# Optimization experiments

Measured on AMD Instinct MI355X. Metric: run time of the kernel, lower is better.

Reference implementation:

```python
import jax, jax.numpy as jnp
import numpy as np

D_MODEL = 1024; D_STATE = 64; HEADDIM = 64; EXPAND = 2
D_INNER = EXPAND * D_MODEL            # 2048
NHEADS = D_INNER // HEADDIM           # 32
NGROUPS = 1
GN = NGROUPS * D_STATE                # 64
CONV_DIM = D_INNER + 2 * (2 * GN)     # 2304
D_IN_PROJ = 2 * D_INNER + 2 * (2 * GN) + 2 * NHEADS  # 4416
K_SP = 7; K_TP = 4; CHUNK = 256
BATCH = 2; FRAMES = 8; SPATIAL = 256; SEQLEN = SPATIAL * FRAMES  # 2048


def silu(x):
    return x * jax.nn.sigmoid(x)


def flip_frames(x, f):
    # 'b (l f) d -> b l f d' flip frame axis, flatten back
    b, L, d = x.shape
    return x.reshape(b, L // f, f, d)[:, :, ::-1, :].reshape(b, L, d)


def depthwise_conv1d(x, w, b, pad):
    # x: (N, L, C), w: (C, K) depthwise, pad=(lo,hi) -> (N, L_out, C)
    y = jax.lax.conv_general_dilated(
        jnp.transpose(x, (0, 2, 1)), w[:, None, :], (1,), [pad],
        feature_group_count=w.shape[0])
    return jnp.transpose(y + b[None, :, None], (0, 2, 1))


def setup_inputs():
    rng = np.random.default_rng(0)
    f32 = lambda *s: jnp.asarray(rng.standard_normal(s), jnp.float32)
    # dt_bias init exactly as in the torch module
    dt = np.exp(rng.random(NHEADS) * (np.log(0.1) - np.log(0.001)) + np.log(0.001))
    dt = np.clip(dt, 1e-4, None)
    inv_dt = dt + np.log(-np.expm1(-dt))
    return {
        "u": f32(BATCH, SEQLEN, D_MODEL),
        "in_proj_w": f32(D_IN_PROJ, D_MODEL) * 0.02,
        "conv_sp_w": f32(CONV_DIM, K_SP) * 0.2,
        "conv_sp_b": f32(CONV_DIM) * 0.02,
        "conv_tp_w": f32(CONV_DIM, K_TP) * 0.2,
        "conv_tp_b": f32(CONV_DIM) * 0.02,
        "dt_bias": jnp.asarray(inv_dt, jnp.float32),
        "A_log": jnp.zeros((NHEADS,), jnp.float32),
        "D": jnp.ones((NHEADS,), jnp.float32),
        "fc_D_w": f32(NHEADS, D_INNER) * 0.02,
        "norm_w": jnp.ones((D_INNER,), jnp.float32),
        "out_proj_w": f32(D_MODEL, D_INNER) * 0.02,
        "num_frames": FRAMES,
    }


def chunked_scan(xh, dt, A, Bm, Cm, sp, cs):
    # xh:(R,L,h,p) dt:(R,L,h) Bm,Cm:(R,L,n). ngroups=1.
    # seq_idx semantics: rows [0:b) one segment; rows [b:2b) reset every sp tokens.
    R, L, H, P = xh.shape
    nch = L // cs
    b = R // 2
    xch = xh.reshape(R, nch, cs, H, P)
    dtc = jnp.transpose(dt.reshape(R, nch, cs, H), (0, 1, 3, 2))   # (R,nch,h,cs)
    Bch = Bm.reshape(R, nch, cs, D_STATE)
    Cch = Cm.reshape(R, nch, cs, D_STATE)
    a = dtc * A[None, None, :, None]                               # negative logs
    cum = jnp.cumsum(a, axis=-1)                                   # inclusive
    mask = jnp.tril(jnp.ones((cs, cs), bool))
    seg = cum[..., :, None] - cum[..., None, :]                    # (R,nch,h,t,s)
    Lmat = jnp.where(mask, jnp.exp(jnp.where(mask, seg, 0.0)), 0.0)
    CB = jnp.einsum('rctn,rcsn->rcts', Cch, Bch)
    M = CB[:, :, None] * Lmat * dtc[:, :, :, None, :]
    Y_intra = jnp.einsum('rchts,rcshp->rcthp', M, xch)
    # chunk-final states and cross-chunk recurrence
    G = jnp.exp(cum[..., -1:] - cum) * dtc                         # (R,nch,h,cs)
    S_chunk = jnp.einsum('rchs,rcshp,rcsn->rchpn', G, xch, Bch)
    chunk_decay = jnp.exp(cum[..., -1])                            # (R,nch,h)
    cidx = jnp.arange(nch)
    rb = (cidx > 0) & ((cidx * cs) % sp == 0)
    resetc = jnp.concatenate([jnp.zeros((b, nch), bool),
                              jnp.broadcast_to(rb, (b, nch))], axis=0)

    def cstep(S, inp):
        dec, Sc, r = inp
        S = jnp.where(r[:, None, None, None], 0.0, S)
        prev = S
        S = dec[:, :, None, None] * S + Sc
        return S, prev

    S0 = jnp.zeros((R, H, P, D_STATE), xh.dtype)
    _, prevs = jax.lax.scan(
        cstep, S0,
        (jnp.transpose(chunk_decay, (1, 0, 2)),
         jnp.transpose(S_chunk, (1, 0, 2, 3, 4)),
         resetc.T))
    prev_states = jnp.transpose(prevs, (1, 0, 2, 3, 4))            # (R,nch,h,p,n)
    Y_inter = jnp.einsum('rcht,rctn,rchpn->rcthp', jnp.exp(cum), Cch, prev_states)
    return (Y_intra + Y_inter).reshape(R, L, H, P)


def reference(u, in_proj_w, conv_sp_w, conv_sp_b, conv_tp_w, conv_tp_b,
              dt_bias, A_log, D, fc_D_w, norm_w, out_proj_w, num_frames):
    batch, seqlen, _ = u.shape
    f = num_frames
    sp = seqlen // f
    zxbcdt = u @ in_proj_w.T
    z = zxbcdt[..., :D_INNER]
    xBC = zxbcdt[..., D_INNER:D_INNER + CONV_DIM]
    dt_raw = zxbcdt[..., D_INNER + CONV_DIM:]
    dt = jnp.concatenate([dt_raw[..., :NHEADS],
                          flip_frames(dt_raw[..., NHEADS:], f)], axis=0)
    dt = jax.nn.softplus(dt + dt_bias)                             # (2b,L,h)
    A = -jnp.exp(A_log)
    # spatial depthwise conv over spatial dim per frame ('same' pad) + SiLU
    xBC = xBC.reshape(batch, sp, f, CONV_DIM).transpose(0, 2, 1, 3).reshape(batch * f, sp, CONV_DIM)
    xBC = silu(depthwise_conv1d(xBC, conv_sp_w, conv_sp_b, (K_SP // 2, K_SP // 2)))
    # causal temporal depthwise conv over frame dim per spatial location + SiLU
    xBC = xBC.reshape(batch, f, sp, CONV_DIM).transpose(0, 2, 1, 3).reshape(batch * sp, f, CONV_DIM)
    xBC = silu(depthwise_conv1d(xBC, conv_tp_w, conv_tp_b, (K_TP - 1, 0)))
    xBC = xBC.reshape(batch, seqlen, CONV_DIM)
    x = xBC[..., :D_INNER]
    BC = xBC[..., D_INNER:]
    x_orig = x
    x2 = jnp.concatenate([x, flip_frames(x, f)], axis=0)
    BC2 = jnp.concatenate([BC[..., :2 * GN], flip_frames(BC[..., 2 * GN:], f)], axis=0)
    Bm, Cm = BC2[..., :GN], BC2[..., GN:]
    xh = x2.reshape(2 * batch, seqlen, NHEADS, HEADDIM)
    y = chunked_scan(xh, dt, A, Bm, Cm, sp, CHUNK)                 # (2b,L,h,p)
    y_fwd = y[:batch].reshape(batch, seqlen, D_INNER)
    y_rev = y[batch:].reshape(batch, sp, f, D_INNER)
    # roll-by-one with zeroed first position (fwd: token axis, rev: spatial axis)
    y_fwd = jnp.concatenate([jnp.zeros_like(y_fwd[:, :1]), y_fwd[:, :-1]], axis=1)
    y_rev = jnp.concatenate([jnp.zeros_like(y_rev[:, :1]), y_rev[:, :-1]], axis=1)
    y_rev = y_rev[:, :, ::-1, :].reshape(batch, seqlen, D_INNER)
    x_res = x_orig * jnp.repeat(x_orig @ fc_D_w.T + D, HEADDIM, axis=-1)
    y = y_fwd + y_rev + x_res
    # gated RMSNorm (norm_before_gate=True): rmsnorm(y)*w*silu(z)
    y = y * jax.lax.rsqrt(jnp.mean(jnp.square(y), axis=-1, keepdims=True) + 1e-5)
    y = y * norm_w * silu(z)
    return y @ out_proj_w.T
```

## Files before the change

### kernel.cpp

```cpp
#include <hip/hip_runtime.h>
#include <hip/hip_bf16.h>
#include <math.h>

#define D_STATE   64
#define HEADDIM   64
#define D_INNER   2048
#define NHEADS    32
#define GN        64
#define CONV_DIM  2304
#define D_IN_PROJ 4416
#define ZLD       4352
#define K_SP      7
#define K_TP      4
#define CHUNK     256
#define BATCHN    2
#define FRAMES    8
#define SPATIAL   256
#define SEQLEN    2048
#define NCH       8
#define MTOT      4096

typedef __attribute__((ext_vector_type(8))) short short8;
typedef __attribute__((ext_vector_type(8))) unsigned short ushort8v;
typedef __attribute__((ext_vector_type(4))) float floatx4;

__device__ __forceinline__ float silu_f(float x) { return x / (1.f + __expf(-x)); }
__device__ __forceinline__ int flip_l(int l) { return (l & ~7) | (7 - (l & 7)); }
__device__ __forceinline__ unsigned short f2bf(float f) {
  unsigned int u = __float_as_uint(f);
  unsigned int r = (u + 0x7fffu + ((u >> 16) & 1u)) >> 16;
  return (unsigned short)r;
}
__device__ __forceinline__ float bf2f(unsigned short s) {
  return __uint_as_float(((unsigned int)s) << 16);
}
__device__ __forceinline__ unsigned int cvtpk_bf16(float lo, float hi) {
  unsigned int r;
  asm("v_cvt_pk_bf16_f32 %0, %1, %2" : "=v"(r) : "v"(lo), "v"(hi));
  return r;
}
typedef union { short8 v; unsigned int u[4]; } s8u;
__device__ __forceinline__ void gload_lds16(const unsigned short* g, unsigned short* l) {
  __builtin_amdgcn_global_load_lds((const __attribute__((address_space(1))) void*)g,
                                   (__attribute__((address_space(3))) void*)l, 16, 0, 0);
}

__global__ __launch_bounds__(256) void cast3_bf16_kernel(const float* __restrict__ a,
                                                         unsigned short* __restrict__ oa,
                                                         int na,
                                                         const float* __restrict__ b,
                                                         unsigned short* __restrict__ ob,
                                                         int nb,
                                                         const float* __restrict__ c,
                                                         unsigned short* __restrict__ oc) {
  int bid = blockIdx.x;
  const float* in;
  unsigned short* out;
  size_t blk;
  if (bid < na)            { in = a; out = oa; blk = bid; }
  else if (bid < na + nb)  { in = b; out = ob; blk = bid - na; }
  else                     { in = c; out = oc; blk = bid - na - nb; }
  size_t i = (blk * 256 + threadIdx.x) * 4;
  float4 v = *(const float4*)(in + i);
  ushort4 o;
  o.x = f2bf(v.x); o.y = f2bf(v.y); o.z = f2bf(v.z); o.w = f2bf(v.w);
  *(ushort4*)(out + i) = o;
}

__global__ __launch_bounds__(256) void gemm_bk64_bf16out(
    const unsigned short* __restrict__ A, int lda,
    const unsigned short* __restrict__ B, int ldb,
    unsigned short* __restrict__ C, int ldc, int K) {
  __shared__ unsigned short As[128 * 64];
  __shared__ unsigned short Bs[128 * 64];
  const int tid = threadIdx.x;
  const int lane = tid & 63;
  const int w = tid >> 6;
  const int bid = blockIdx.x;
  const int xcd = bid & 7;
  const int rp  = bid >> 3;
  const int px  = rp % 17;
  const int py  = rp / 17;
  const int m0 = ((xcd >> 1) * 8 + py) * 128;
  const int n0 = ((xcd & 1) * 17 + px) * 128;
  const int wm = (w >> 1) * 64;
  const int wn = (w & 1) * 64;
  const int lrow = lane >> 3;
  const int lperm = lane & 7;
  floatx4 acc[4][4] = {};
  for (int k0 = 0; k0 < K; k0 += 64) {
#pragma unroll
    for (int j = 0; j < 8; ++j) {
      int g = j * 4 + w;
      if (g < 16) {
        int row = g * 8 + lrow;
        int cg = (lperm ^ (row & 7)) * 8;
        gload_lds16(A + (size_t)(m0 + row) * lda + k0 + cg, &As[g * 512]);
      } else {
        int gb = g - 16;
        int row = gb * 8 + lrow;
        int cg = (lperm ^ (row & 7)) * 8;
        gload_lds16(B + (size_t)(n0 + row) * ldb + k0 + cg, &Bs[gb * 512]);
      }
    }
    __syncthreads();
    const int fr = lane & 15;
    const int kq = (lane >> 4) * 8;
#pragma unroll
    for (int kk = 0; kk < 64; kk += 32) {
      int u = (kk + kq) >> 3;
      short8 af[4], bfr[4];
#pragma unroll
      for (int i = 0; i < 4; ++i) {
        int row = wm + i * 16 + fr;
        af[i] = *(const short8*)&As[(row * 8 + (u ^ (row & 7))) * 8];
      }
#pragma unroll
      for (int j = 0; j < 4; ++j) {
        int row = wn + j * 16 + fr;
        bfr[j] = *(const short8*)&Bs[(row * 8 + (u ^ (row & 7))) * 8];
      }
#pragma unroll
      for (int i = 0; i < 4; ++i)
#pragma unroll
        for (int j = 0; j < 4; ++j)
          acc[i][j] = __builtin_amdgcn_mfma_f32_16x16x32_bf16(af[i], bfr[j], acc[i][j], 0, 0, 0);
    }
    __syncthreads();
  }
  const int fr = lane & 15;
  const int rg = (lane >> 4) * 4;
  unsigned short* Ew = &As[w * 1024];
  const int rr = lane >> 3;
  const int c8 = (lane & 7) * 8;
#pragma unroll
  for (int i = 0; i < 4; ++i) {
#pragma unroll
    for (int q = 0; q < 4; ++q)
#pragma unroll
      for (int j = 0; j < 4; ++j)
        Ew[(rg + q) * 64 + j * 16 + fr] = f2bf(acc[i][j][q]);
    ushort8v v0 = *(const ushort8v*)&Ew[rr * 64 + c8];
    ushort8v v1 = *(const ushort8v*)&Ew[(rr + 8) * 64 + c8];
    *(ushort8v*)(C + (size_t)(m0 + wm + i * 16 + rr) * ldc + n0 + wn + c8) = v0;
    *(ushort8v*)(C + (size_t)(m0 + wm + i * 16 + rr + 8) * ldc + n0 + wn + c8) = v1;
  }
}

__global__ __launch_bounds__(256) void gemm_m64_f32(
    const unsigned short* __restrict__ A, int lda,
    const unsigned short* __restrict__ B, int ldb,
    float* __restrict__ C, int ldc, int K) {
  __shared__ unsigned short As[64 * 64];
  __shared__ unsigned short Bs[128 * 64];
  const int tid = threadIdx.x;
  const int lane = tid & 63;
  const int w = tid >> 6;
  const int bid = blockIdx.x;
  const int xcd = bid & 7;
  const int q8  = bid >> 3;
  const int rsel = q8 >> 5;
  const int rp   = q8 & 31;
  const int reg  = xcd + 8 * rsel;
  const int m0 = ((reg >> 1) * 8 + (rp >> 2)) * 64;
  const int n0 = ((reg & 1) * 4 + (rp & 3)) * 128;
  const int wm = (w >> 1) * 32;
  const int wn = (w & 1) * 64;
  const int lrow = lane >> 3;
  const int lperm = lane & 7;
  floatx4 acc[2][4] = {};
  for (int k0 = 0; k0 < K; k0 += 64) {
#pragma unroll
    for (int j = 0; j < 6; ++j) {
      int g = j * 4 + w;
      if (g < 8) {
        int row = g * 8 + lrow;
        int cg = (lperm ^ (row & 7)) * 8;
        gload_lds16(A + (size_t)(m0 + row) * lda + k0 + cg, &As[g * 512]);
      } else {
        int gb = g - 8;
        int row = gb * 8 + lrow;
        int cg = (lperm ^ (row & 7)) * 8;
        gload_lds16(B + (size_t)(n0 + row) * ldb + k0 + cg, &Bs[gb * 512]);
      }
    }
    __syncthreads();
    const int fr = lane & 15;
    const int kq = (lane >> 4) * 8;
#pragma unroll
    for (int kk = 0; kk < 64; kk += 32) {
      int u = (kk + kq) >> 3;
      short8 af[2], bfr[4];
#pragma unroll
      for (int i = 0; i < 2; ++i) {
        int row = wm + i * 16 + fr;
        af[i] = *(const short8*)&As[(row * 8 + (u ^ (row & 7))) * 8];
      }
#pragma unroll
      for (int j = 0; j < 4; ++j) {
        int row = wn + j * 16 + fr;
        bfr[j] = *(const short8*)&Bs[(row * 8 + (u ^ (row & 7))) * 8];
      }
#pragma unroll
      for (int i = 0; i < 2; ++i)
#pragma unroll
        for (int j = 0; j < 4; ++j)
          acc[i][j] = __builtin_amdgcn_mfma_f32_16x16x32_bf16(af[i], bfr[j], acc[i][j], 0, 0, 0);
    }
    __syncthreads();
  }
  const int col = lane & 15;
  const int rg = (lane >> 4) * 4;
#pragma unroll
  for (int i = 0; i < 2; ++i)
#pragma unroll
    for (int j = 0; j < 4; ++j)
#pragma unroll
      for (int r = 0; r < 4; ++r)
        C[(size_t)(m0 + wm + i * 16 + rg + r) * ldc + (n0 + wn + j * 16 + col)] = acc[i][j][r];
}

__global__ __launch_bounds__(256) void gemm_ts_mfma(
    const unsigned short* __restrict__ A, int lda,
    const float* __restrict__ B, int ldb,
    float* __restrict__ C, int ldc, int N, int K) {
  __shared__ float red[4][1024];
  const int tid = threadIdx.x;
  const int lane = tid & 63;
  const int w = tid >> 6;
  const int m0 = blockIdx.x * 16;
  const int fr = lane & 15;
  const int kq = (lane >> 4) * 8;
  const int nt = N >> 4;
  const int kseg = K >> 2;
  const int k0 = w * kseg;
  floatx4 acc[4] = {};
  for (int k = k0; k < k0 + kseg; k += 32) {
    short8 af = *(const short8*)(A + (size_t)(m0 + fr) * lda + k + kq);
    for (int j = 0; j < nt; ++j) {
      const float* bp = B + (size_t)(j * 16 + fr) * ldb + k + kq;
      float4 b0 = *(const float4*)bp;
      float4 b1 = *(const float4*)(bp + 4);
      short8 bf8;
      bf8[0] = (short)f2bf(b0.x); bf8[1] = (short)f2bf(b0.y);
      bf8[2] = (short)f2bf(b0.z); bf8[3] = (short)f2bf(b0.w);
      bf8[4] = (short)f2bf(b1.x); bf8[5] = (short)f2bf(b1.y);
      bf8[6] = (short)f2bf(b1.z); bf8[7] = (short)f2bf(b1.w);
      acc[j] = __builtin_amdgcn_mfma_f32_16x16x32_bf16(af, bf8, acc[j], 0, 0, 0);
    }
  }
  const int rg = (lane >> 4) * 4;
  for (int j = 0; j < nt; ++j)
#pragma unroll
    for (int q = 0; q < 4; ++q)
      red[w][j * 256 + (rg + q) * 16 + fr] = acc[j][q];
  __syncthreads();
  const int entries = nt * 256;
  for (int e = tid; e < entries; e += 256) {
    float s = red[0][e] + red[1][e] + red[2][e] + red[3][e];
    int j = e >> 8, idx = e & 255, row = idx >> 4, col = idx & 15;
    C[(size_t)(m0 + row) * ldc + j * 16 + col] = s;
  }
}

__global__ __launch_bounds__(256) void dtscan_kernel(const float* __restrict__ DTraw,
                                                     const float* __restrict__ dt_bias,
                                                     const float* __restrict__ A_log,
                                                     float* __restrict__ DTt,
                                                     float* __restrict__ CUMS) {
  __shared__ float sc[256];
  int tid = threadIdx.x;
  int idx = blockIdx.x * 256 + tid;
  int l  = idx & 2047;
  int rh = idx >> 11;
  int h  = rh & 31;
  int r  = rh >> 5;
  int bi = r & 1;
  int ls = (r < 2) ? l : flip_l(l);
  int ch = (r < 2) ? h : NHEADS + h;
  float raw = DTraw[((size_t)bi * SEQLEN + ls) * 64 + ch] + dt_bias[h];
  float dtv = (raw > 20.f) ? raw : log1pf(__expf(raw));
  DTt[idx] = dtv;
  float A = -__expf(A_log[h]);
  float run = dtv * A;
  sc[tid] = run;
  __syncthreads();
#pragma unroll
  for (int ofs = 1; ofs < 256; ofs <<= 1) {
    float add = (tid >= ofs) ? sc[tid - ofs] : 0.f;
    __syncthreads();
    run += add;
    sc[tid] = run;
    __syncthreads();
  }
  CUMS[idx] = run;
}

__global__ __launch_bounds__(256) void conv_fused2_kernel(const unsigned short* __restrict__ Zb,
                                                          const float* __restrict__ wsp,
                                                          const float* __restrict__ bsp,
                                                          const float* __restrict__ wtp,
                                                          const float* __restrict__ btp,
                                                          unsigned short* __restrict__ XTb) {
  __shared__ float4 xsl[8][8][32];
  const int tid = threadIdx.x;
  const int g  = tid & 31;
  const int fr = tid >> 5;
  const int c  = blockIdx.x * 128 + g * 4;
  const int s0 = blockIdx.y * 8;
  const int bi = blockIdx.z;
  float wsp_r[4][K_SP];
#pragma unroll
  for (int ch = 0; ch < 4; ++ch)
#pragma unroll
    for (int j = 0; j < K_SP; ++j) wsp_r[ch][j] = wsp[(c + ch) * K_SP + j];
  float4 bsp4 = *(const float4*)(bsp + c);
  float4 z[14];
#pragma unroll
  for (int i = 0; i < 14; ++i) {
    int ss = s0 - 3 + i;
    if (0 <= ss && ss < SPATIAL) {
      ushort4 v = *(const ushort4*)(Zb + ((size_t)bi * SEQLEN + (ss*8 + fr)) * ZLD + D_INNER + c);
      z[i] = make_float4(bf2f(v.x), bf2f(v.y), bf2f(v.z), bf2f(v.w));
    } else {
      z[i] = make_float4(0.f, 0.f, 0.f, 0.f);
    }
  }
#pragma unroll
  for (int so = 0; so < 8; ++so) {
    float4 a = bsp4;
#pragma unroll
    for (int j = 0; j < K_SP; ++j) {
      a.x += wsp_r[0][j] * z[so + j].x;
      a.y += wsp_r[1][j] * z[so + j].y;
      a.z += wsp_r[2][j] * z[so + j].z;
      a.w += wsp_r[3][j] * z[so + j].w;
    }
    a.x = silu_f(a.x); a.y = silu_f(a.y); a.z = silu_f(a.z); a.w = silu_f(a.w);
    xsl[fr][so][g] = a;
  }
  __syncthreads();
  float wtp_r[4][K_TP];
#pragma unroll
  for (int ch = 0; ch < 4; ++ch)
#pragma unroll
    for (int j = 0; j < K_TP; ++j) wtp_r[ch][j] = wtp[(c + ch) * K_TP + j];
  float4 btp4 = *(const float4*)(btp + c);
#pragma unroll
  for (int so = 0; so < 8; ++so) {
    float4 t = btp4;
#pragma unroll
    for (int j = 0; j < K_TP; ++j) {
      int ff = fr + j - (K_TP - 1);
      if (ff >= 0) {
        float4 xv = xsl[ff][so][g];
        t.x += wtp_r[0][j] * xv.x;
        t.y += wtp_r[1][j] * xv.y;
        t.z += wtp_r[2][j] * xv.z;
        t.w += wtp_r[3][j] * xv.w;
      }
    }
    ushort4 o;
    o.x = f2bf(silu_f(t.x)); o.y = f2bf(silu_f(t.y));
    o.z = f2bf(silu_f(t.z)); o.w = f2bf(silu_f(t.w));
    *(ushort4*)(XTb + ((size_t)bi * SEQLEN + ((s0 + so)*8 + fr)) * CONV_DIM + c) = o;
  }
}

__global__ __launch_bounds__(256) void cb_kernel(const unsigned short* __restrict__ XTb,
                                                 float* __restrict__ CBs) {
  int tid = threadIdx.x;
  int lane = tid & 63;
  int w = tid >> 6;
  int t0 = (blockIdx.x & 3) * 64;
  int s0 = (blockIdx.x >> 2) * 64;
  if (s0 > t0) return;
  int c = blockIdx.y;
  int r = blockIdx.z;
  int bi = r & 1;
  int bOff = D_INNER + ((r < 2) ? 0 : 2*GN);
  int cOff = bOff + GN;
  const int fr = lane & 15;
  const int kq = (lane >> 4) * 8;
  int Lc = c * CHUNK + t0 + w * 16 + fr;
  if (r >= 2) Lc = flip_l(Lc);
  const unsigned short* crow = XTb + ((size_t)bi*SEQLEN + Lc)*CONV_DIM + cOff;
  short8 af0 = *(const short8*)(crow + kq);
  short8 af1 = *(const short8*)(crow + 32 + kq);
  floatx4 acc[4] = {};
#pragma unroll
  for (int j = 0; j < 4; ++j) {
    int Ls = c * CHUNK + s0 + j * 16 + fr;
    if (r >= 2) Ls = flip_l(Ls);
    const unsigned short* brow = XTb + ((size_t)bi*SEQLEN + Ls)*CONV_DIM + bOff;
    short8 bf0 = *(const short8*)(brow + kq);
    short8 bf1 = *(const short8*)(brow + 32 + kq);
    acc[j] = __builtin_amdgcn_mfma_f32_16x16x32_bf16(af0, bf0, acc[j], 0, 0, 0);
    acc[j] = __builtin_amdgcn_mfma_f32_16x16x32_bf16(af1, bf1, acc[j], 0, 0, 0);
  }
  const int col = lane & 15;
  const int rg = (lane >> 4) * 4;
  size_t base = (((size_t)r*NCH + c) * CHUNK) * CHUNK;
#pragma unroll
  for (int j = 0; j < 4; ++j)
#pragma unroll
    for (int q = 0; q < 4; ++q)
      CBs[base + (size_t)(t0 + w*16 + rg + q)*CHUNK + (s0 + j*16 + col)] = acc[j][q];
}

__global__ __launch_bounds__(256) void chunk_state_kernel(const unsigned short* __restrict__ XTb,
                                                          const float* __restrict__ DTt,
                                                          const float* __restrict__ CUMS,
                                                          float* __restrict__ SCH) {
  __shared__ unsigned short Xs[64 * 136];
  __shared__ unsigned short Bs[64 * 136];
  __shared__ float gs[CHUNK];
  int tid = threadIdx.x;
  int lane = tid & 63;
  int w = tid >> 6;
  int c = blockIdx.x;
  int h = blockIdx.y;
  int r = blockIdx.z;
  int bi = r;
  int rh = r * NHEADS + h;
  float cl = CUMS[(size_t)rh*SEQLEN + c*CHUNK + 255];
  gs[tid] = __expf(cl - CUMS[(size_t)rh*SEQLEN + c*CHUNK + tid]) * DTt[(size_t)rh*SEQLEN + c*CHUNK + tid];
  const int fr = lane & 15;
  const int kq = (lane >> 4) * 8;
  const int sr = tid >> 3;
  const int p0 = (tid & 7) * 8;
  const int swz = (tid & 7) << 3;
  floatx4 acc[4] = {};
  for (int half = 0; half < 2; ++half) {
    __syncthreads();
#pragma unroll
    for (int P = 0; P < 4; ++P) {
      int s = P * 32 + sr;
      int l = c*CHUNK + half*128 + s;
      const unsigned short* row = XTb + ((size_t)bi*SEQLEN + l)*CONV_DIM;
      ushort8v xv = *(const ushort8v*)(row + h*HEADDIM + p0);
      ushort8v bv = *(const ushort8v*)(row + D_INNER + p0);
      float g = gs[half*128 + s];
      int cswz = s ^ swz;
#pragma unroll
      for (int q = 0; q < 8; ++q) {
        Xs[(p0 + q) * 136 + cswz] = f2bf(g * bf2f(xv[q]));
        Bs[(p0 + q) * 136 + cswz] = bv[q];
      }
    }
    __syncthreads();
#pragma unroll
    for (int sl = 0; sl < 4; ++sl) {
      int s0 = sl * 32;
      int Ra = w*16 + fr;
      short8 af = *(const short8*)&Xs[Ra * 136 + ((s0 + kq) ^ (((Ra >> 3) & 7) << 3))];
#pragma unroll
      for (int j = 0; j < 4; ++j) {
        int Rb = j*16 + fr;
        short8 bf8 = *(const short8*)&Bs[Rb * 136 + ((s0 + kq) ^ (((Rb >> 3) & 7) << 3))];
        acc[j] = __builtin_amdgcn_mfma_f32_16x16x32_bf16(af, bf8, acc[j], 0, 0, 0);
      }
    }
  }
  const int col = lane & 15;
  const int rg = (lane >> 4) * 4;
  size_t base = (((size_t)r*NCH + c)*NHEADS + h) * (size_t)(HEADDIM*D_STATE);
#pragma unroll
  for (int j = 0; j < 4; ++j)
#pragma unroll
    for (int q = 0; q < 4; ++q)
      SCH[base + (size_t)(w*16 + rg + q)*D_STATE + j*16 + col] = acc[j][q];
}

__global__ __launch_bounds__(256) void state_combine_kernel(const float* __restrict__ SCH,
                                                            const float* __restrict__ CUMS,
                                                            float* __restrict__ SPREV) {
  int bid = blockIdx.x;
  int pq = bid & 3;
  int h = (bid >> 2) & 31;
  int r = bid >> 7;
  int tid = threadIdx.x;
  int p = pq*16 + (tid >> 4);
  int n = (tid & 15) * 4;
  float4 S = make_float4(0.f, 0.f, 0.f, 0.f);
  for (int c = 0; c < NCH; ++c) {
    size_t off = ((((size_t)r*NCH + c)*NHEADS + h)*HEADDIM + p)*D_STATE + n;
    *(float4*)(SPREV + off) = S;
    float dec = __expf(CUMS[((size_t)r*NHEADS + h)*SEQLEN + c*CHUNK + 255]);
    float4 v = *(const float4*)(SCH + off);
    S.x = dec*S.x + v.x; S.y = dec*S.y + v.y;
    S.z = dec*S.z + v.z; S.w = dec*S.w + v.w;
  }
}

#define YS_ED(S0)                                                              \
  float edv[8];                                                                \
  { float4 e0_ = *(const float4*)&ecd[(S0) + kq];                              \
    float4 e1_ = *(const float4*)&ecd[(S0) + kq + 4];                          \
    edv[0]=e0_.x; edv[1]=e0_.y; edv[2]=e0_.z; edv[3]=e0_.w;                    \
    edv[4]=e1_.x; edv[5]=e1_.y; edv[6]=e1_.z; edv[7]=e1_.w; }

#define YS_BFR(S0)                                                             \
  short8 bfr[4];                                                               \
  _Pragma("unroll")                                                            \
  for (int j = 0; j < 4; ++j) {                                                \
    int R = j * 16 + fr;                                                       \
    bfr[j] = *(const short8*)&Xt[R * 264 + (((S0) + kq) ^ (((R >> 3) & 7) << 3))]; \
  }

#define YS_MFMA4(AF, ACCROW)                                                   \
  _Pragma("unroll")                                                            \
  for (int j = 0; j < 4; ++j)                                                  \
    ACCROW[j] = __builtin_amdgcn_mfma_f32_16x16x32_bf16(AF, bfr[j], ACCROW[j], 0, 0, 0);

#define YS_AF_NOMASK(C0, C1, E)                                                \
  { af_.u[0] = cvtpk_bf16(C0.x*(E)*edv[0], C0.y*(E)*edv[1]);                   \
    af_.u[1] = cvtpk_bf16(C0.z*(E)*edv[2], C0.w*(E)*edv[3]);                   \
    af_.u[2] = cvtpk_bf16(C1.x*(E)*edv[4], C1.y*(E)*edv[5]);                   \
    af_.u[3] = cvtpk_bf16(C1.z*(E)*edv[6], C1.w*(E)*edv[7]); }

#define YS_AF_MASK(C0, C1, E, TROW)                                            \
  { float wz[8] = {C0.x,C0.y,C0.z,C0.w,C1.x,C1.y,C1.z,C1.w};                   \
    _Pragma("unroll")                                                          \
    for (int jj = 0; jj < 8; ++jj) {                                           \
      float t_ = wz[jj]*(E)*edv[jj];                                           \
      wz[jj] = (kq + jj <= (TROW)) ? t_ : 0.f; }                               \
    af_.u[0]=cvtpk_bf16(wz[0],wz[1]); af_.u[1]=cvtpk_bf16(wz[2],wz[3]);        \
    af_.u[2]=cvtpk_bf16(wz[4],wz[5]); af_.u[3]=cvtpk_bf16(wz[6],wz[7]); }

#define YS_STRIP(KS, E2, ACC)                                                  \
  {                                                                            \
    const int t0s_ = (KS) * 32;                                                \
    const float* cbr0 = CBs + cbbase + (size_t)(t0s_ + fr) * CHUNK + kq;       \
    const float* cbr1 = cbr0 + (size_t)16 * CHUNK;                             \
    float4 a0 = *(const float4*)cbr0;                                          \
    float4 a1 = *(const float4*)(cbr0 + 4);                                    \
    float4 b0 = *(const float4*)cbr1;                                          \
    float4 b1 = *(const float4*)(cbr1 + 4);                                    \
    for (int sl = 0; sl < (KS); ++sl) {                                        \
      int s0 = sl * 32;                                                        \
      float4 na0 = *(const float4*)(cbr0 + s0 + 32);                           \
      float4 na1 = *(const float4*)(cbr0 + s0 + 36);                           \
      float4 nb0 = *(const float4*)(cbr1 + s0 + 32);                           \
      float4 nb1 = *(const float4*)(cbr1 + s0 + 36);                           \
      YS_ED(s0); YS_BFR(s0);                                                   \
      s8u af_;                                                                 \
      YS_AF_NOMASK(a0, a1, (E2)[0]);                                           \
      YS_MFMA4(af_.v, ACC[0]);                                                 \
      YS_AF_NOMASK(b0, b1, (E2)[1]);                                           \
      YS_MFMA4(af_.v, ACC[1]);                                                 \
      a0 = na0; a1 = na1; b0 = nb0; b1 = nb1;                                  \
    }                                                                          \
    {                                                                          \
      int s0 = (KS) * 32;                                                      \
// ... 129 lines not shown
                                                      const float* __restrict__ norm_w,
                                                      unsigned short* __restrict__ YPb) {
  __shared__ float red4[4];
  int row = blockIdx.x;
  int bi = row >> 11;
  int l = row & 2047;
  int s = l >> 3, fr = l & 7;
  int tid = threadIdx.x;
  int d0 = tid * 8;
  const unsigned short* yf = (l >= 1) ? Y + ((size_t)bi*SEQLEN + (l-1))*D_INNER + d0 : nullptr;
  const unsigned short* yr = (s >= 1) ? Y + ((size_t)(2+bi)*SEQLEN + ((s-1)*8 + (7-fr)))*D_INNER + d0 : nullptr;
  const unsigned short* xr = XTb + ((size_t)row)*CONV_DIM + d0;
  float fcv = FCD[(size_t)row*NHEADS + (d0 >> 6)] + Dp[d0 >> 6];
  ushort8v xv8 = *(const ushort8v*)xr;
  float v[8];
#pragma unroll
  for (int q = 0; q < 8; ++q) v[q] = bf2f(xv8[q]) * fcv;
  if (yf) {
    ushort8v a = *(const ushort8v*)yf;
#pragma unroll
    for (int q = 0; q < 8; ++q) v[q] += bf2f(a[q]);
  }
  if (yr) {
    ushort8v a = *(const ushort8v*)yr;
#pragma unroll
    for (int q = 0; q < 8; ++q) v[q] += bf2f(a[q]);
  }
  float ss = 0.f;
#pragma unroll
  for (int q = 0; q < 8; ++q) ss += v[q] * v[q];
#pragma unroll
  for (int d = 1; d < 64; d <<= 1) ss += __shfl_xor(ss, d, 64);
  if ((tid & 63) == 0) red4[tid >> 6] = ss;
  __syncthreads();
  float tot = red4[0] + red4[1] + red4[2] + red4[3];
  float rs = rsqrtf(tot / (float)D_INNER + 1e-5f);
  ushort8v zv8 = *(const ushort8v*)(Zb + ((size_t)row)*ZLD + d0);
  float4 nw0 = *(const float4*)(norm_w + d0);
  float4 nw1 = *(const float4*)(norm_w + d0 + 4);
  float nw[8] = {nw0.x,nw0.y,nw0.z,nw0.w,nw1.x,nw1.y,nw1.z,nw1.w};
  ushort8v o;
#pragma unroll
  for (int q = 0; q < 8; ++q)
    o[q] = f2bf(v[q] * rs * nw[q] * silu_f(bf2f(zv8[q])));
  *(ushort8v*)(YPb + (size_t)row*D_INNER + d0) = o;
}

extern "C" void kernel_launch(void* const* d_in, const int* in_sizes, int n_in,
                              void* d_out, int out_size, void* d_ws, size_t ws_size,
                              hipStream_t stream) {
  (void)in_sizes; (void)n_in; (void)out_size; (void)ws_size;
  const float* u          = (const float*)d_in[0];
  const float* in_proj_w  = (const float*)d_in[1];
  const float* conv_sp_w  = (const float*)d_in[2];
  const float* conv_sp_b  = (const float*)d_in[3];
  const float* conv_tp_w  = (const float*)d_in[4];
  const float* conv_tp_b  = (const float*)d_in[5];
  const float* dt_bias    = (const float*)d_in[6];
  const float* A_log      = (const float*)d_in[7];
  const float* Dp         = (const float*)d_in[8];
  const float* fc_D_w     = (const float*)d_in[9];
  const float* norm_w     = (const float*)d_in[10];
  const float* out_proj_w = (const float*)d_in[11];
  float* out = (float*)d_out;
  float* ws = (float*)d_ws;

  float* Z     = ws;
  float* SH    = Z     + 17825792ULL;
  float* XT    = SH    + 9437184ULL;
  float* DTt   = XT    + 9437184ULL;
  float* Yb    = DTt   + 262144ULL;
  float* SPREV = Yb    + 16777216ULL;
  float* FCD   = SPREV + 2097152ULL;
  float* DTraw = FCD   + 131072ULL;
  float* CUMS  = DTraw + 262144ULL;

  unsigned short* Zb   = (unsigned short*)Z;
  unsigned short* XTb  = (unsigned short*)XT;
  unsigned short* Yb16 = (unsigned short*)Yb;
  unsigned short* Ub   = (unsigned short*)Yb;
  unsigned short* Wb   = (unsigned short*)Yb + 4194304ULL;
  float* SCH = Yb + 8388608ULL;
  unsigned short* Wob = (unsigned short*)(Yb + 10485760ULL);
  unsigned short* YPb = (unsigned short*)SH;

  cast3_bf16_kernel<<<10496, 256, 0, stream>>>(u, Ub, 4096, in_proj_w, Wb, 4352,
                                               out_proj_w, Wob);
  gemm_bk64_bf16out<<<dim3(1088), 256, 0, stream>>>(Ub, 1024, Wb, 1024, Zb, ZLD, 1024);
  gemm_ts_mfma<<<256, 256, 0, stream>>>(Ub, 1024, in_proj_w + 4352ULL*1024, 1024,
                                        DTraw, 64, 64, 1024);
  dtscan_kernel<<<1024, 256, 0, stream>>>(DTraw, dt_bias, A_log, DTt, CUMS);
  conv_fused2_kernel<<<dim3(18, 32, 2), 256, 0, stream>>>(Zb, conv_sp_w, conv_sp_b,
                                                          conv_tp_w, conv_tp_b, XTb);
  gemm_ts_mfma<<<256, 256, 0, stream>>>(XTb, CONV_DIM, fc_D_w, 2048,
                                        FCD, 32, 32, 2048);
  cb_kernel<<<dim3(16, 8, 4), 256, 0, stream>>>(XTb, SH);
  chunk_state_kernel<<<dim3(NCH, NHEADS, 2), 256, 0, stream>>>(XTb, DTt, CUMS, SCH);
  state_combine_kernel<<<256, 256, 0, stream>>>(SCH, CUMS, SPREV);
  yscan_kernel<<<dim3(1024), 256, 0, stream>>>(XTb, DTt, CUMS, SH, SPREV, Yb16);
  combine_kernel<<<4096, 256, 0, stream>>>(Yb16, XTb, FCD, Dp, Zb, norm_w, YPb);
  gemm_m64_f32<<<dim3(512), 256, 0, stream>>>(YPb, 2048, Wob, 2048, out, 1024, 2048);
}
```

Measured before the change: 321.8 us.

## Merge independent launches into horizontally fused kernels and pre-cast small weights to bf16

Independent kernels run as one launch each, with branches chosen by block index. The dt-scan and conv kernels become one launch, and chunk_state, cb (with the empty upper-triangle blocks dropped from the grid) and the fc_D skinny GEMM become another. The dt and fc_D weight rows are now cast to bf16 in the shared cast kernel, so the skinny GEMMs load bf16 directly instead of converting fp32 in their inner loop. This removes launch gaps and lets independent work overlap, at the cost of mixed shared-memory and register footprints within one kernel, which may lower occupancy.

```diff
diff --git a/kernel.cpp b/kernel.cpp
--- a/kernel.cpp
+++ b/kernel.cpp
@@ -45,21 +45,25 @@
                                    (__attribute__((address_space(3))) void*)l, 16, 0, 0);
 }
 
-__global__ __launch_bounds__(256) void cast3_bf16_kernel(const float* __restrict__ a,
+__global__ __launch_bounds__(256) void cast4_bf16_kernel(const float* __restrict__ a,
                                                          unsigned short* __restrict__ oa,
                                                          int na,
                                                          const float* __restrict__ b,
                                                          unsigned short* __restrict__ ob,
                                                          int nb,
                                                          const float* __restrict__ c,
-                                                         unsigned short* __restrict__ oc) {
+                                                         unsigned short* __restrict__ oc,
+                                                         int nc,
+                                                         const float* __restrict__ d,
+                                                         unsigned short* __restrict__ od) {
   int bid = blockIdx.x;
   const float* in;
   unsigned short* out;
   size_t blk;
-  if (bid < na)            { in = a; out = oa; blk = bid; }
-  else if (bid < na + nb)  { in = b; out = ob; blk = bid - na; }
-  else                     { in = c; out = oc; blk = bid - na - nb; }
+  if (bid < na)                 { in = a; out = oa; blk = bid; }
+  else if (bid < na + nb)       { in = b; out = ob; blk = bid - na; }
+  else if (bid < na + nb + nc)  { in = c; out = oc; blk = bid - na - nb; }
+  else                          { in = d; out = od; blk = bid - na - nb - nc; }
   size_t i = (blk * 256 + threadIdx.x) * 4;
   float4 v = *(const float4*)(in + i);
   ushort4 o;
@@ -220,15 +224,13 @@
         C[(size_t)(m0 + wm + i * 16 + rg + r) * ldc + (n0 + wn + j * 16 + col)] = acc[i][j][r];
 }
 
-__global__ __launch_bounds__(256) void gemm_ts_mfma(
-    const unsigned short* __restrict__ A, int lda,
-    const float* __restrict__ B, int ldb,
-    float* __restrict__ C, int ldc, int N, int K) {
-  __shared__ float red[4][1024];
+__device__ __forceinline__ void ts_body_bf16(const unsigned short* __restrict__ A, int lda,
+                                             const unsigned short* __restrict__ B, int ldb,
+                                             float* __restrict__ C, int ldc, int N, int K,
+                                             int m0, float* red) {
   const int tid = threadIdx.x;
   const int lane = tid & 63;
   const int w = tid >> 6;
-  const int m0 = blockIdx.x * 16;
   const int fr = lane & 15;
   const int kq = (lane >> 4) * 8;
   const int nt = N >> 4;
@@ -238,14 +240,7 @@
   for (int k = k0; k < k0 + kseg; k += 32) {
     short8 af = *(const short8*)(A + (size_t)(m0 + fr) * lda + k + kq);
     for (int j = 0; j < nt; ++j) {
-      const float* bp = B + (size_t)(j * 16 + fr) * ldb + k + kq;
-      float4 b0 = *(const float4*)bp;
-      float4 b1 = *(const float4*)(bp + 4);
-      short8 bf8;
-      bf8[0] = (short)f2bf(b0.x); bf8[1] = (short)f2bf(b0.y);
-      bf8[2] = (short)f2bf(b0.z); bf8[3] = (short)f2bf(b0.w);
-      bf8[4] = (short)f2bf(b1.x); bf8[5] = (short)f2bf(b1.y);
-      bf8[6] = (short)f2bf(b1.z); bf8[7] = (short)f2bf(b1.w);
+      short8 bf8 = *(const short8*)(B + (size_t)(j * 16 + fr) * ldb + k + kq);
       acc[j] = __builtin_amdgcn_mfma_f32_16x16x32_bf16(af, bf8, acc[j], 0, 0, 0);
     }
   }
@@ -253,223 +248,238 @@
   for (int j = 0; j < nt; ++j)
 #pragma unroll
     for (int q = 0; q < 4; ++q)
-      red[w][j * 256 + (rg + q) * 16 + fr] = acc[j][q];
+      red[w * 1024 + j * 256 + (rg + q) * 16 + fr] = acc[j][q];
   __syncthreads();
   const int entries = nt * 256;
   for (int e = tid; e < entries; e += 256) {
-    float s = red[0][e] + red[1][e] + red[2][e] + red[3][e];
+    float s = red[e] + red[1024 + e] + red[2048 + e] + red[3072 + e];
     int j = e >> 8, idx = e & 255, row = idx >> 4, col = idx & 15;
     C[(size_t)(m0 + row) * ldc + j * 16 + col] = s;
   }
 }
 
-__global__ __launch_bounds__(256) void dtscan_kernel(const float* __restrict__ DTraw,
-                                                     const float* __restrict__ dt_bias,
-                                                     const float* __restrict__ A_log,
-                                                     float* __restrict__ DTt,
-                                                     float* __restrict__ CUMS) {
-  __shared__ float sc[256];
-  int tid = threadIdx.x;
-  int idx = blockIdx.x * 256 + tid;
-  int l  = idx & 2047;
-  int rh = idx >> 11;
-  int h  = rh & 31;
-  int r  = rh >> 5;
-  int bi = r & 1;
-  int ls = (r < 2) ? l : flip_l(l);
-  int ch = (r < 2) ? h : NHEADS + h;
-  float raw = DTraw[((size_t)bi * SEQLEN + ls) * 64 + ch] + dt_bias[h];
-  float dtv = (raw > 20.f) ? raw : log1pf(__expf(raw));
-  DTt[idx] = dtv;
-  float A = -__expf(A_log[h]);
-  float run = dtv * A;
-  sc[tid] = run;
-  __syncthreads();
-#pragma unroll
-  for (int ofs = 1; ofs < 256; ofs <<= 1) {
-    float add = (tid >= ofs) ? sc[tid - ofs] : 0.f;
-    __syncthreads();
-    run += add;
+__global__ __launch_bounds__(256) void gemm_ts_bf16(
+    const unsigned short* __restrict__ A, int lda,
+    const unsigned short* __restrict__ B, int ldb,
+    float* __restrict__ C, int ldc, int N, int K) {
+  __shared__ float red[4 * 1024];
+  ts_body_bf16(A, lda, B, ldb, C, ldc, N, K, blockIdx.x * 16, red);
+}
+
+__global__ __launch_bounds__(256) void fused_dtconv_kernel(
+    const float* __restrict__ DTraw, const float* __restrict__ dt_bias,
+    const float* __restrict__ A_log, float* __restrict__ DTt, float* __restrict__ CUMS,
+    const unsigned short* __restrict__ Zb, const float* __restrict__ wsp,
+    const float* __restrict__ bsp, const float* __restrict__ wtp,
+    const float* __restrict__ btp, unsigned short* __restrict__ XTb) {
+  __shared__ __align__(16) char smem[32768];
+  const int tid = threadIdx.x;
+  if (blockIdx.x < 1024) {
+    float* sc = (float*)smem;
+    int idx = blockIdx.x * 256 + tid;
+    int l  = idx & 2047;
+    int rh = idx >> 11;
+    int h  = rh & 31;
+    int r  = rh >> 5;
+    int bi = r & 1;
+    int ls = (r < 2) ? l : flip_l(l);
+    int ch = (r < 2) ? h : NHEADS + h;
+    float raw = DTraw[((size_t)bi * SEQLEN + ls) * 64 + ch] + dt_bias[h];
+    float dtv = (raw > 20.f) ? raw : log1pf(__expf(raw));
+    DTt[idx] = dtv;
+    float A = -__expf(A_log[h]);
+    float run = dtv * A;
     sc[tid] = run;
     __syncthreads();
-  }
-  CUMS[idx] = run;
-}
-
-__global__ __launch_bounds__(256) void conv_fused2_kernel(const unsigned short* __restrict__ Zb,
-                                                          const float* __restrict__ wsp,
-                                                          const float* __restrict__ bsp,
-                                                          const float* __restrict__ wtp,
-                                                          const float* __restrict__ btp,
-                                                          unsigned short* __restrict__ XTb) {
-  __shared__ float4 xsl[8][8][32];
+#pragma unroll
+    for (int ofs = 1; ofs < 256; ofs <<= 1) {
+      float add = (tid >= ofs) ? sc[tid - ofs] : 0.f;
+      __syncthreads();
+      run += add;
+      sc[tid] = run;
+      __syncthreads();
+    }
+    CUMS[idx] = run;
+  } else {
+    typedef float4 xsl_t[8][32];
+    xsl_t* xsl = (xsl_t*)smem;
+    int bid = blockIdx.x - 1024;
+    const int bx = bid % 18;
+    const int by = (bid / 18) & 31;
+    const int bz = bid / 576;
+    const int g  = tid & 31;
+    const int fr = tid >> 5;
+    const int c  = bx * 128 + g * 4;
+    const int s0 = by * 8;
+    const int bi = bz;
+    float wsp_r[4][K_SP];
+#pragma unroll
+    for (int ch = 0; ch < 4; ++ch)
+#pragma unroll
+      for (int j = 0; j < K_SP; ++j) wsp_r[ch][j] = wsp[(c + ch) * K_SP + j];
+    float4 bsp4 = *(const float4*)(bsp + c);
+    float4 z[14];
+#pragma unroll
+    for (int i = 0; i < 14; ++i) {
+      int ss = s0 - 3 + i;
+      if (0 <= ss && ss < SPATIAL) {
+        ushort4 v = *(const ushort4*)(Zb + ((size_t)bi * SEQLEN + (ss*8 + fr)) * ZLD + D_INNER + c);
+        z[i] = make_float4(bf2f(v.x), bf2f(v.y), bf2f(v.z), bf2f(v.w));
+      } else {
+        z[i] = make_float4(0.f, 0.f, 0.f, 0.f);
+      }
+    }
+#pragma unroll
+    for (int so = 0; so < 8; ++so) {
+      float4 a = bsp4;
+#pragma unroll
+      for (int j = 0; j < K_SP; ++j) {
+        a.x += wsp_r[0][j] * z[so + j].x;
+        a.y += wsp_r[1][j] * z[so + j].y;
+        a.z += wsp_r[2][j] * z[so + j].z;
+        a.w += wsp_r[3][j] * z[so + j].w;
+      }
+      a.x = silu_f(a.x); a.y = silu_f(a.y); a.z = silu_f(a.z); a.w = silu_f(a.w);
+      xsl[fr][so][g] = a;
+    }
+    __syncthreads();
+    float wtp_r[4][K_TP];
+#pragma unroll
+    for (int ch = 0; ch < 4; ++ch)
+#pragma unroll
+      for (int j = 0; j < K_TP; ++j) wtp_r[ch][j] = wtp[(c + ch) * K_TP + j];
+    float4 btp4 = *(const float4*)(btp + c);
+#pragma unroll
+    for (int so = 0; so < 8; ++so) {
+      float4 t = btp4;
+#pragma unroll
+      for (int j = 0; j < K_TP; ++j) {
+        int ff = fr + j - (K_TP - 1);
+        if (ff >= 0) {
+          float4 xv = xsl[ff][so][g];
+          t.x += wtp_r[0][j] * xv.x;
+          t.y += wtp_r[1][j] * xv.y;
+          t.z += wtp_r[2][j] * xv.z;
+          t.w += wtp_r[3][j] * xv.w;
+        }
+      }
+      ushort4 o;
+      o.x = f2bf(silu_f(t.x)); o.y = f2bf(silu_f(t.y));
+      o.z = f2bf(silu_f(t.z)); o.w = f2bf(silu_f(t.w));
+      *(ushort4*)(XTb + ((size_t)bi * SEQLEN + ((s0 + so)*8 + fr)) * CONV_DIM + c) = o;
+    }
+  }
+}
+
+__global__ __launch_bounds__(256) void fused_post_kernel(
+    const unsigned short* __restrict__ XTb, const float* __restrict__ DTt,
+    const float* __restrict__ CUMS, float* __restrict__ CBs,
+    float* __restrict__ SCH, const unsigned short* __restrict__ FCDWb,
+    float* __restrict__ FCD) {
+  __shared__ __align__(16) char smem[35840];
   const int tid = threadIdx.x;
-  const int g  = tid & 31;
-  const int fr = tid >> 5;
-  const int c  = blockIdx.x * 128 + g * 4;
-  const int s0 = blockIdx.y * 8;
-  const int bi = blockIdx.z;
-  float wsp_r[4][K_SP];
-#pragma unroll
-  for (int ch = 0; ch < 4; ++ch)
-#pragma unroll
-    for (int j = 0; j < K_SP; ++j) wsp_r[ch][j] = wsp[(c + ch) * K_SP + j];
-  float4 bsp4 = *(const float4*)(bsp + c);
-  float4 z[14];
-#pragma unroll
-  for (int i = 0; i < 14; ++i) {
-    int ss = s0 - 3 + i;
-    if (0 <= ss && ss < SPATIAL) {
-      ushort4 v = *(const ushort4*)(Zb + ((size_t)bi * SEQLEN + (ss*8 + fr)) * ZLD + D_INNER + c);
-      z[i] = make_float4(bf2f(v.x), bf2f(v.y), bf2f(v.z), bf2f(v.w));
-    } else {
-      z[i] = make_float4(0.f, 0.f, 0.f, 0.f);
-    }
-  }
-#pragma unroll
-  for (int so = 0; so < 8; ++so) {
-    float4 a = bsp4;
-#pragma unroll
-    for (int j = 0; j < K_SP; ++j) {
-      a.x += wsp_r[0][j] * z[so + j].x;
-      a.y += wsp_r[1][j] * z[so + j].y;
-      a.z += wsp_r[2][j] * z[so + j].z;
-      a.w += wsp_r[3][j] * z[so + j].w;
-    }
-    a.x = silu_f(a.x); a.y = silu_f(a.y); a.z = silu_f(a.z); a.w = silu_f(a.w);
-    xsl[fr][so][g] = a;
-  }
-  __syncthreads();
-  float wtp_r[4][K_TP];
-#pragma unroll
-  for (int ch = 0; ch < 4; ++ch)
-#pragma unroll
-    for (int j = 0; j < K_TP; ++j) wtp_r[ch][j] = wtp[(c + ch) * K_TP + j];
-  float4 btp4 = *(const float4*)(btp + c);
-#pragma unroll
-  for (int so = 0; so < 8; ++so) {
-    float4 t = btp4;
-#pragma unroll
-    for (int j = 0; j < K_TP; ++j) {
-      int ff = fr + j - (K_TP - 1);
-      if (ff >= 0) {
-        float4 xv = xsl[ff][so][g];
-        t.x += wtp_r[0][j] * xv.x;
-        t.y += wtp_r[1][j] * xv.y;
-        t.z += wtp_r[2][j] * xv.z;
-        t.w += wtp_r[3][j] * xv.w;
-      }
-    }
-    ushort4 o;
-    o.x = f2bf(silu_f(t.x)); o.y = f2bf(silu_f(t.y));
-    o.z = f2bf(silu_f(t.z)); o.w = f2bf(silu_f(t.w));
-    *(ushort4*)(XTb + ((size_t)bi * SEQLEN + ((s0 + so)*8 + fr)) * CONV_DIM + c) = o;
-  }
-}
-
-__global__ __launch_bounds__(256) void cb_kernel(const unsigned short* __restrict__ XTb,
-                                                 float* __restrict__ CBs) {
-  int tid = threadIdx.x;
-  int lane = tid & 63;
-  int w = tid >> 6;
-  int t0 = (blockIdx.x & 3) * 64;
-  int s0 = (blockIdx.x >> 2) * 64;
-  if (s0 > t0) return;
-  int c = blockIdx.y;
-  int r = blockIdx.z;
-  int bi = r & 1;
-  int bOff = D_INNER + ((r < 2) ? 0 : 2*GN);
-  int cOff = bOff + GN;
-  const int fr = lane & 15;
-  const int kq = (lane >> 4) * 8;
-  int Lc = c * CHUNK + t0 + w * 16 + fr;
-  if (r >= 2) Lc = flip_l(Lc);
-  const unsigned short* crow = XTb + ((size_t)bi*SEQLEN + Lc)*CONV_DIM + cOff;
-  short8 af0 = *(const short8*)(crow + kq);
-  short8 af1 = *(const short8*)(crow + 32 + kq);
-  floatx4 acc[4] = {};
-#pragma unroll
-  for (int j = 0; j < 4; ++j) {
-    int Ls = c * CHUNK + s0 + j * 16 + fr;
-    if (r >= 2) Ls = flip_l(Ls);
-    const unsigned short* brow = XTb + ((size_t)bi*SEQLEN + Ls)*CONV_DIM + bOff;
-    short8 bf0 = *(const short8*)(brow + kq);
-    short8 bf1 = *(const short8*)(brow + 32 + kq);
-    acc[j] = __builtin_amdgcn_mfma_f32_16x16x32_bf16(af0, bf0, acc[j], 0, 0, 0);
-    acc[j] = __builtin_amdgcn_mfma_f32_16x16x32_bf16(af1, bf1, acc[j], 0, 0, 0);
-  }
-  const int col = lane & 15;
-  const int rg = (lane >> 4) * 4;
-  size_t base = (((size_t)r*NCH + c) * CHUNK) * CHUNK;
-#pragma unroll
-  for (int j = 0; j < 4; ++j)
-#pragma unroll
-    for (int q = 0; q < 4; ++q)
-      CBs[base + (size_t)(t0 + w*16 + rg + q)*CHUNK + (s0 + j*16 + col)] = acc[j][q];
-}
-
-__global__ __launch_bounds__(256) void chunk_state_kernel(const unsigned short* __restrict__ XTb,
-                                                          const float* __restrict__ DTt,
-                                                          const float* __restrict__ CUMS,
-                                                          float* __restrict__ SCH) {
-  __shared__ unsigned short Xs[64 * 136];
-  __shared__ unsigned short Bs[64 * 136];
-  __shared__ float gs[CHUNK];
-  int tid = threadIdx.x;
-  int lane = tid & 63;
-  int w = tid >> 6;
-  int c = blockIdx.x;
-  int h = blockIdx.y;
-  int r = blockIdx.z;
-  int bi = r;
-  int rh = r * NHEADS + h;
-  float cl = CUMS[(size_t)rh*SEQLEN + c*CHUNK + 255];
-  gs[tid] = __expf(cl - CUMS[(size_t)rh*SEQLEN + c*CHUNK + tid]) * DTt[(size_t)rh*SEQLEN + c*CHUNK + tid];
-  const int fr = lane & 15;
-  const int kq = (lane >> 4) * 8;
-  const int sr = tid >> 3;
-  const int p0 = (tid & 7) * 8;
-  const int swz = (tid & 7) << 3;
-  floatx4 acc[4] = {};
-  for (int half = 0; half < 2; ++half) {
-    __syncthreads();
-#pragma unroll
-    for (int P = 0; P < 4; ++P) {
-      int s = P * 32 + sr;
-      int l = c*CHUNK + half*128 + s;
-      const unsigned short* row = XTb + ((size_t)bi*SEQLEN + l)*CONV_DIM;
-      ushort8v xv = *(const ushort8v*)(row + h*HEADDIM + p0);
-      ushort8v bv = *(const ushort8v*)(row + D_INNER + p0);
-      float g = gs[half*128 + s];
-      int cswz = s ^ swz;
-#pragma unroll
-      for (int q = 0; q < 8; ++q) {
-        Xs[(p0 + q) * 136 + cswz] = f2bf(g * bf2f(xv[q]));
-        Bs[(p0 + q) * 136 + cswz] = bv[q];
-      }
-    }
-    __syncthreads();
-#pragma unroll
-    for (int sl = 0; sl < 4; ++sl) {
-      int s0 = sl * 32;
-      int Ra = w*16 + fr;
-      short8 af = *(const short8*)&Xs[Ra * 136 + ((s0 + kq) ^ (((Ra >> 3) & 7) << 3))];
-#pragma unroll
-      for (int j = 0; j < 4; ++j) {
-        int Rb = j*16 + fr;
-        short8 bf8 = *(const short8*)&Bs[Rb * 136 + ((s0 + kq) ^ (((Rb >> 3) & 7) << 3))];
-        acc[j] = __builtin_amdgcn_mfma_f32_16x16x32_bf16(af, bf8, acc[j], 0, 0, 0);
-      }
-    }
-  }
-  const int col = lane & 15;
-  const int rg = (lane >> 4) * 4;
-  size_t base = (((size_t)r*NCH + c)*NHEADS + h) * (size_t)(HEADDIM*D_STATE);
-#pragma unroll
-  for (int j = 0; j < 4; ++j)
-#pragma unroll
-    for (int q = 0; q < 4; ++q)
-      SCH[base + (size_t)(w*16 + rg + q)*D_STATE + j*16 + col] = acc[j][q];
+  const int bidx = blockIdx.x;
+  const int lane = tid & 63;
+  const int w = tid >> 6;
+  if (bidx < 512) {
+    unsigned short* Xs = (unsigned short*)smem;
+    unsigned short* Bsm = Xs + 64 * 136;
+    float* gs = (float*)(Bsm + 64 * 136);
+    int c = bidx & 7;
+    int h = (bidx >> 3) & 31;
+    int r = bidx >> 8;
+    int bi = r;
+    int rh = r * NHEADS + h;
+    float cl = CUMS[(size_t)rh*SEQLEN + c*CHUNK + 255];
+    gs[tid] = __expf(cl - CUMS[(size_t)rh*SEQLEN + c*CHUNK + tid]) * DTt[(size_t)rh*SEQLEN + c*CHUNK + tid];
+    const int fr = lane & 15;
+    const int kq = (lane >> 4) * 8;
+    const int sr = tid >> 3;
+    const int p0 = (tid & 7) * 8;
+    const int swz = (tid & 7) << 3;
+    floatx4 acc[4] = {};
+    for (int half = 0; half < 2; ++half) {
+      __syncthreads();
+#pragma unroll
+      for (int P = 0; P < 4; ++P) {
+        int s = P * 32 + sr;
+        int l = c*CHUNK + half*128 + s;
+        const unsigned short* row = XTb + ((size_t)bi*SEQLEN + l)*CONV_DIM;
+        ushort8v xv = *(const ushort8v*)(row + h*HEADDIM + p0);
+        ushort8v bv = *(const ushort8v*)(row + D_INNER + p0);
+        float g = gs[half*128 + s];
+        int cswz = s ^ swz;
+#pragma unroll
+        for (int q = 0; q < 8; ++q) {
+          Xs[(p0 + q) * 136 + cswz] = f2bf(g * bf2f(xv[q]));
+          Bsm[(p0 + q) * 136 + cswz] = bv[q];
+        }
+      }
+      __syncthreads();
+#pragma unroll
+      for (int sl = 0; sl < 4; ++sl) {
+        int s0 = sl * 32;
+        int Ra = w*16 + fr;
+        short8 af = *(const short8*)&Xs[Ra * 136 + ((s0 + kq) ^ (((Ra >> 3) & 7) << 3))];
+#pragma unroll
+        for (int j = 0; j < 4; ++j) {
+          int Rb = j*16 + fr;
+          short8 bf8 = *(const short8*)&Bsm[Rb * 136 + ((s0 + kq) ^ (((Rb >> 3) & 7) << 3))];
+          acc[j] = __builtin_amdgcn_mfma_f32_16x16x32_bf16(af, bf8, acc[j], 0, 0, 0);
+        }
+      }
+    }
+    const int col = lane & 15;
+    const int rg = (lane >> 4) * 4;
+    size_t base = (((size_t)r*NCH + c)*NHEADS + h) * (size_t)(HEADDIM*D_STATE);
+#pragma unroll
+    for (int j = 0; j < 4; ++j)
+#pragma unroll
+      for (int q = 0; q < 4; ++q)
+        SCH[base + (size_t)(w*16 + rg + q)*D_STATE + j*16 + col] = acc[j][q];
+  } else if (bidx < 832) {
+    const int TT0[10] = {0,1,1,2,2,2,3,3,3,3};
+    const int SS0[10] = {0,0,1,0,1,2,0,1,2,3};
+    int t = bidx - 512;
+    int tt = t % 10;
+    int rc = t / 10;
+    int c = rc & 7;
+    int r = rc >> 3;
+    int t0 = TT0[tt] * 64;
+    int s0 = SS0[tt] * 64;
+    int bi = r & 1;
+    int bOff = D_INNER + ((r < 2) ? 0 : 2*GN);
+    int cOff = bOff + GN;
+    const int fr = lane & 15;
+    const int kq = (lane >> 4) * 8;
+    int Lc = c * CHUNK + t0 + w * 16 + fr;
+    if (r >= 2) Lc = flip_l(Lc);
+    const unsigned short* crow = XTb + ((size_t)bi*SEQLEN + Lc)*CONV_DIM + cOff;
+    short8 af0 = *(const short8*)(crow + kq);
+    short8 af1 = *(const short8*)(crow + 32 + kq);
+    floatx4 acc[4] = {};
+#pragma unroll
+    for (int j = 0; j < 4; ++j) {
+      int Ls = c * CHUNK + s0 + j * 16 + fr;
+      if (r >= 2) Ls = flip_l(Ls);
+      const unsigned short* brow = XTb + ((size_t)bi*SEQLEN + Ls)*CONV_DIM + bOff;
+      short8 bf0 = *(const short8*)(brow + kq);
+      short8 bf1 = *(const short8*)(brow + 32 + kq);
+      acc[j] = __builtin_amdgcn_mfma_f32_16x16x32_bf16(af0, bf0, acc[j], 0, 0, 0);
+      acc[j] = __builtin_amdgcn_mfma_f32_16x16x32_bf16(af1, bf1, acc[j], 0, 0, 0);
+    }
+    const int col = lane & 15;
+    const int rg = (lane >> 4) * 4;
+    size_t base = (((size_t)r*NCH + c) * CHUNK) * CHUNK;
+#pragma unroll
+    for (int j = 0; j < 4; ++j)
+#pragma unroll
+      for (int q = 0; q < 4; ++q)
+        CBs[base + (size_t)(t0 + w*16 + rg + q)*CHUNK + (s0 + j*16 + col)] = acc[j][q];
+  } else {
+    ts_body_bf16(XTb, CONV_DIM, FCDWb, 2048, FCD, 32, 32, 2048,
+                 (bidx - 832) * 16, (float*)smem);
+  }
 }
 
 __global__ __launch_bounds__(256) void state_combine_kernel(const float* __restrict__ SCH,
@@ -765,20 +775,18 @@
   unsigned short* Wb   = (unsigned short*)Yb + 4194304ULL;
   float* SCH = Yb + 8388608ULL;
   unsigned short* Wob = (unsigned short*)(Yb + 10485760ULL);
+  unsigned short* FCDWb = (unsigned short*)(Yb + 11534336ULL);
   unsigned short* YPb = (unsigned short*)SH;
 
-  cast3_bf16_kernel<<<10496, 256, 0, stream>>>(u, Ub, 4096, in_proj_w, Wb, 4352,
-                                               out_proj_w, Wob);
+  cast4_bf16_kernel<<<10624, 256, 0, stream>>>(u, Ub, 4096, in_proj_w, Wb, 4416,
+                                               out_proj_w, Wob, 2048, fc_D_w, FCDWb);
   gemm_bk64_bf16out<<<dim3(1088), 256, 0, stream>>>(Ub, 1024, Wb, 1024, Zb, ZLD, 1024);
-  gemm_ts_mfma<<<256, 256, 0, stream>>>(Ub, 1024, in_proj_w + 4352ULL*1024, 1024,
+  gemm_ts_bf16<<<256, 256, 0, stream>>>(Ub, 1024, Wb + 4352ULL*1024, 1024,
                                         DTraw, 64, 64, 1024);
-  dtscan_kernel<<<1024, 256, 0, stream>>>(DTraw, dt_bias, A_log, DTt, CUMS);
-  conv_fused2_kernel<<<dim3(18, 32, 2), 256, 0, stream>>>(Zb, conv_sp_w, conv_sp_b,
-                                                          conv_tp_w, conv_tp_b, XTb);
-  gemm_ts_mfma<<<256, 256, 0, stream>>>(XTb, CONV_DIM, fc_D_w, 2048,
-                                        FCD, 32, 32, 2048);
-  cb_kernel<<<dim3(16, 8, 4), 256, 0, stream>>>(XTb, SH);
-  chunk_state_kernel<<<dim3(NCH, NHEADS, 2), 256, 0, stream>>>(XTb, DTt, CUMS, SCH);
+  fused_dtconv_kernel<<<2176, 256, 0, stream>>>(DTraw, dt_bias, A_log, DTt, CUMS,
+                                                Zb, conv_sp_w, conv_sp_b,
+                                                conv_tp_w, conv_tp_b, XTb);
+  fused_post_kernel<<<1088, 256, 0, stream>>>(XTb, DTt, CUMS, SH, SCH, FCDWb, FCD);
   state_combine_kernel<<<256, 256, 0, stream>>>(SCH, CUMS, SPREV);
   yscan_kernel<<<dim3(1024), 256, 0, stream>>>(XTb, DTt, CUMS, SH, SPREV, Yb16);
   combine_kernel<<<4096, 256, 0, stream>>>(Yb16, XTb, FCD, Dp, Zb, norm_w, YPb);
```

Result: faster. 289.9 us (-9.9%).
